# Optimization experiments

Measured on AMD Instinct MI355X. Metric: run time of the kernel, lower is better.

Reference implementation:

```python
import jax, jax.numpy as jnp
import numpy as np

IN_FEATURES = 4096
OUT_FEATURES = 4096
BLOCK_SIZE = 4096
NUM_BLOCKS = 4096
CODEBOOK_SIZE = 256
TOTAL_WEIGHTS = OUT_FEATURES * IN_FEATURES


def setup_inputs() -> dict:
    key = jax.random.key(0)
    k_x, k_cb, k_b, k_idx = jax.random.split(key, 4)
    x = jax.random.normal(k_x, (4, 2048, IN_FEATURES), dtype=jnp.float32)
    codebook = jax.random.normal(k_cb, (NUM_BLOCKS, CODEBOOK_SIZE), dtype=jnp.float32)
    bias = jax.random.normal(k_b, (OUT_FEATURES,), dtype=jnp.float32)
    indices = jax.random.randint(k_idx, (NUM_BLOCKS, BLOCK_SIZE), 0, CODEBOOK_SIZE, dtype=jnp.int64)
    return {"x": x, "codebook": codebook, "bias": bias, "indices": indices}


def reference(x, codebook, bias, indices):
    # weight = codebook[block_idx, indices] : per-block gather of codebook entries
    # codebook: [num_blocks, codebook_size], indices: [num_blocks, block_size]
    w_blocks = jnp.take_along_axis(codebook, indices, axis=1)  # [num_blocks, block_size]
    weight = w_blocks.reshape(-1)[:TOTAL_WEIGHTS].reshape(OUT_FEATURES, IN_FEATURES)
    # F.linear: x @ weight.T + bias
    return jnp.einsum("bsi,oi->bso", x, weight) + bias
```

## Files before the change

kernel.cpp:

```cpp
#include <hip/hip_runtime.h>

typedef __bf16 bf16x8 __attribute__((ext_vector_type(8)));
typedef float f32x4 __attribute__((ext_vector_type(4)));
typedef unsigned short u16x8 __attribute__((ext_vector_type(8)));
typedef int i32x4 __attribute__((ext_vector_type(4)));

#define M_TOT 8192
#define K_TOT 4096
#define N_TOT 4096
#define BM 256
#define BN 256
#define BK 64
#define NT (K_TOT / BK)

__device__ __forceinline__ unsigned short f2bf(float f) {
  union { float f; unsigned int u; } v; v.f = f;
  unsigned int u = v.u;
  return (unsigned short)((u + 0x7FFFu + ((u >> 16) & 1u)) >> 16);
}

__global__ __launch_bounds__(256) void prep(const float* __restrict__ cb,
                                            const int* __restrict__ idx,
                                            const float* __restrict__ X,
                                            unsigned short* __restrict__ Wb,
                                            unsigned short* __restrict__ Xc) {
  const int b = blockIdx.x;
  if (b < 8192) {
    size_t base = ((size_t)b * 256 + threadIdx.x) * 8;
    const float* crow = cb + ((base >> 12) << 8);
    i32x4 i0 = *(const i32x4*)(idx + base);
    i32x4 i1 = *(const i32x4*)(idx + base + 4);
    u16x8 o;
#pragma unroll
    for (int j = 0; j < 4; ++j) { o[j] = f2bf(crow[i0[j]]); o[4 + j] = f2bf(crow[i1[j]]); }
    *(u16x8*)(Wb + base) = o;
  } else {
    size_t base = ((size_t)(b - 8192) * 256 + threadIdx.x) * 8;
    f32x4 a = *(const f32x4*)(X + base);
    f32x4 c = *(const f32x4*)(X + base + 4);
    u16x8 o;
#pragma unroll
    for (int j = 0; j < 4; ++j) { o[j] = f2bf(a[j]); o[4 + j] = f2bf(c[j]); }
    *(u16x8*)(Xc + base) = o;
  }
}

#define GLDS16(g, l)                                                      \
  __builtin_amdgcn_global_load_lds(                                       \
      (__attribute__((address_space(1))) void*)(g),                       \
      (__attribute__((address_space(3))) void*)(l), 16, 0, 0)

__global__ __launch_bounds__(512, 2) void gemm8(const unsigned short* __restrict__ A,
                                                const unsigned short* __restrict__ B,
                                                const float* __restrict__ bias,
                                                float* __restrict__ C) {
  __shared__ __attribute__((aligned(128))) char lds[131072];

  const int tid = threadIdx.x;
  const int lane = tid & 63;
  const int wm = (tid >> 6) >> 2;
  const int wn = (tid >> 6) & 3;
  const int lr = lane & 15;

  const int bid = blockIdx.x;
  const int swz = (bid & 7) * 64 + (bid >> 3);
  const int bm = swz >> 4;
  const int bn = swz & 15;

  const unsigned short* Ap = A + (size_t)bm * BM * K_TOT;
  const unsigned short* Bp = B + (size_t)bn * BN * K_TOT;

  const int srow = tid >> 3;
  const int sgcol = (((tid & 7) * 16) ^ ((srow & 7) << 4)) >> 1;
  const int wavebase = (tid & 448) << 4;

  const int cs0 = (((lane >> 4) << 4)) ^ ((lr & 7) << 4);
  const int cs1 = (64 + ((lane >> 4) << 4)) ^ ((lr & 7) << 4);
  const int rowA0 = (wm * 128 + lr) * 128;
  const int rowB0 = 32768 + (wn * 64 + lr) * 128;

#define RD(off) (*(const bf16x8*)(lds + (off)))
#define STAGE(GB, TK, RB, LOFF)                                               \
  { _Pragma("unroll")                                                         \
    for (int ii = 0; ii < 2; ++ii) {                                          \
      GLDS16((GB) + (size_t)((RB) + ii * 64 + srow) * K_TOT + (TK) + sgcol,   \
             lds + (LOFF) + ii * 8192 + wavebase);                            \
    } }
#define BARRIER()                       \
  {                                     \
    asm volatile("" ::: "memory");      \
    __builtin_amdgcn_s_barrier();       \
    asm volatile("" ::: "memory");      \
  }

#define MFMA_Q(MH, AV, BV)                                                    \
  { __builtin_amdgcn_s_setprio(1);                                            \
    _Pragma("unroll")                                                         \
    for (int r = 0; r < 4; ++r) {                                             \
      _Pragma("unroll")                                                       \
      for (int nf = 0; nf < 4; ++nf)                                          \
        acc[(MH) * 4 + r][nf] = __builtin_amdgcn_mfma_f32_16x16x32_bf16(      \
            AV[r], BV[nf], acc[(MH) * 4 + r][nf], 0, 0, 0);                   \
    }                                                                         \
    __builtin_amdgcn_s_setprio(0); }

#define TILE(T, BO, STG_A, STG_B, VMF, DO_BAR)                                    \
  {                                                                               \
    bf16x8 Aa[4], Ab[4], Ac[4], Ad[4], Bx[4], By[4];                              \
    _Pragma("unroll") for (int r = 0; r < 4; ++r)                                 \
        Aa[r] = RD((BO) + rowA0 + r * 2048 + cs0);                                \
    _Pragma("unroll") for (int n = 0; n < 4; ++n)                                 \
        Bx[n] = RD((BO) + rowB0 + n * 2048 + cs0);                                \
    if (STG_A) STAGE(Ap, ((T) + 1) * BK, 0, ((BO) ^ 65536) + 0);                  \
    _Pragma("unroll") for (int r = 0; r < 4; ++r)                                 \
        Ab[r] = RD((BO) + rowA0 + (4 + r) * 2048 + cs0);                          \
    if (STG_A) STAGE(Ap, ((T) + 1) * BK, 128, ((BO) ^ 65536) + 16384);            \
    MFMA_Q(0, Aa, Bx);                                                            \
    _Pragma("unroll") for (int r = 0; r < 4; ++r)                                 \
        Ac[r] = RD((BO) + rowA0 + r * 2048 + cs1);                                \
    _Pragma("unroll") for (int n = 0; n < 4; ++n)                                 \
        By[n] = RD((BO) + rowB0 + n * 2048 + cs1);                                \
    MFMA_Q(1, Ab, Bx);                                                            \
    asm volatile("s_waitcnt lgkmcnt(0)" ::: "memory");                            \
    BARRIER();                                                                    \
    if (STG_B) STAGE(Bp, ((T) + 2) * BK, 0, (BO) + 32768);                        \
    if (STG_B) STAGE(Bp, ((T) + 2) * BK, 128, (BO) + 49152);                      \
    _Pragma("unroll") for (int r = 0; r < 4; ++r)                                 \
        Ad[r] = RD((BO) + rowA0 + (4 + r) * 2048 + cs1);                          \
    MFMA_Q(0, Ac, By);                                                            \
    MFMA_Q(1, Ad, By);                                                            \
    asm volatile("s_waitcnt vmcnt(" VMF ")" ::: "memory");                        \
    if (DO_BAR) BARRIER();                                                        \
  }

  f32x4 acc[8][4] = {};

  STAGE(Bp, 0, 0, 32768);
  STAGE(Bp, 0, 128, 49152);
  STAGE(Ap, 0, 0, 0);
  STAGE(Ap, 0, 128, 16384);
  STAGE(Bp, BK, 0, 65536 + 32768);
  STAGE(Bp, BK, 128, 65536 + 49152);
  asm volatile("s_waitcnt vmcnt(4)" ::: "memory");
  BARRIER();

  for (int t = 0; t < NT - 2; t += 2) {
    TILE(t,     0,     1, 1, "4", 1);
    TILE(t + 1, 65536, 1, 1, "4", 1);
  }
  TILE(NT - 2, 0,     1, 0, "0", 1);
  TILE(NT - 1, 65536, 0, 0, "0", 0);

  const int lg4 = (lane >> 4) << 2;
#pragma unroll
  for (int nf = 0; nf < 4; ++nf) {
    const int col = bn * BN + wn * 64 + nf * 16 + lr;
    const float bv = bias[col];
#pragma unroll
    for (int mf = 0; mf < 8; ++mf) {
      const int row0 = bm * BM + wm * 128 + mf * 16 + lg4;
      float* cp = C + (size_t)row0 * N_TOT + col;
#pragma unroll
      for (int j = 0; j < 4; ++j) cp[(size_t)j * N_TOT] = acc[mf][nf][j] + bv;
    }
  }
#undef RD
#undef STAGE
#undef BARRIER
#undef MFMA_Q
#undef TILE
}

extern "C" void kernel_launch(void* const* d_in, const int* in_sizes, int n_in,
                              void* d_out, int out_size, void* d_ws, size_t ws_size,
                              hipStream_t stream) {
  const float* x    = (const float*)d_in[0];
  const float* cb   = (const float*)d_in[1];
  const float* bias = (const float*)d_in[2];
  const int*   idx  = (const int*)d_in[3];

  float* out = (float*)d_out;

  unsigned short* Wb = (unsigned short*)d_ws;
  unsigned short* Xc = (unsigned short*)((char*)d_ws + (size_t)N_TOT * K_TOT * 2);

  prep<<<24576, 256, 0, stream>>>(cb, idx, x, Wb, Xc);
  gemm8<<<512, 512, 0, stream>>>(Xc, Wb, bias, out);
}
```

Measured before the change: 275.0 us.

## Restructure GEMM tile into four barrier-fenced quadrant phases with interleaved staging

Reorganizes each K-tile of the bf16 MFMA GEMM into four quadrant phases (M-half x N-half), each loading both K sub-slices of its fragments from LDS, then a barrier-fenced MFMA cluster. Global-to-LDS staging of the next A and B tiles is spread across the phases. The aim is a ping-pong style schedule where the two co-resident workgroups alternate between LDS reads and MFMA bursts, so memory and matrix work overlap. The extra barriers per tile add synchronization overhead, and the register pressure for holding A fragments across phases changes.

```diff
diff --git a/kernel.cpp b/kernel.cpp
--- a/kernel.cpp
+++ b/kernel.cpp
@@ -92,64 +92,84 @@
     __builtin_amdgcn_s_barrier();       \
     asm volatile("" ::: "memory");      \
   }
-
-#define MFMA_Q(MH, AV, BV)                                                    \
+#define LGKM0() asm volatile("s_waitcnt lgkmcnt(0)" ::: "memory")
+
+#define MFMA_Q(MH, NH, AV, BV)                                                \
   { __builtin_amdgcn_s_setprio(1);                                            \
     _Pragma("unroll")                                                         \
     for (int r = 0; r < 4; ++r) {                                             \
       _Pragma("unroll")                                                       \
-      for (int nf = 0; nf < 4; ++nf)                                          \
-        acc[(MH) * 4 + r][nf] = __builtin_amdgcn_mfma_f32_16x16x32_bf16(      \
-            AV[r], BV[nf], acc[(MH) * 4 + r][nf], 0, 0, 0);                   \
+      for (int n2 = 0; n2 < 2; ++n2) {                                        \
+        acc[(MH)*4+r][(NH)*2+n2] = __builtin_amdgcn_mfma_f32_16x16x32_bf16(   \
+            AV[r*2+0], BV[n2*2+0], acc[(MH)*4+r][(NH)*2+n2], 0, 0, 0);        \
+        acc[(MH)*4+r][(NH)*2+n2] = __builtin_amdgcn_mfma_f32_16x16x32_bf16(   \
+            AV[r*2+1], BV[n2*2+1], acc[(MH)*4+r][(NH)*2+n2], 0, 0, 0);        \
+      }                                                                       \
     }                                                                         \
     __builtin_amdgcn_s_setprio(0); }
 
-#define TILE(T, BO, STG_A, STG_B, VMF, DO_BAR)                                    \
+#define TILE(T, BO, STG_A, STG_B, VMF, LAST)                                      \
   {                                                                               \
-    bf16x8 Aa[4], Ab[4], Ac[4], Ad[4], Bx[4], By[4];                              \
-    _Pragma("unroll") for (int r = 0; r < 4; ++r)                                 \
-        Aa[r] = RD((BO) + rowA0 + r * 2048 + cs0);                                \
-    _Pragma("unroll") for (int n = 0; n < 4; ++n)                                 \
-        Bx[n] = RD((BO) + rowB0 + n * 2048 + cs0);                                \
+    bf16x8 Aq[8], A2[8], Bn0[4], Bn1[4];                                          \
+                   \
+    _Pragma("unroll") for (int r = 0; r < 4; ++r) {                               \
+      Aq[r*2+0] = RD((BO) + rowA0 + r * 2048 + cs0);                              \
+      Aq[r*2+1] = RD((BO) + rowA0 + r * 2048 + cs1);                              \
+    }                                                                             \
+    _Pragma("unroll") for (int n = 0; n < 2; ++n) {                               \
+      Bn0[n*2+0] = RD((BO) + rowB0 + n * 2048 + cs0);                             \
+      Bn0[n*2+1] = RD((BO) + rowB0 + n * 2048 + cs1);                             \
+    }                                                                             \
     if (STG_A) STAGE(Ap, ((T) + 1) * BK, 0, ((BO) ^ 65536) + 0);                  \
-    _Pragma("unroll") for (int r = 0; r < 4; ++r)                                 \
-        Ab[r] = RD((BO) + rowA0 + (4 + r) * 2048 + cs0);                          \
+    asm volatile("s_waitcnt lgkmcnt(8)" ::: "memory");                            \
+    BARRIER(); LGKM0();                                                           \
+    MFMA_Q(0, 0, Aq, Bn0);                                                        \
+    BARRIER();                                                                    \
+                               \
+    _Pragma("unroll") for (int n = 0; n < 2; ++n) {                               \
+      Bn1[n*2+0] = RD((BO) + rowB0 + (2 + n) * 2048 + cs0);                       \
+      Bn1[n*2+1] = RD((BO) + rowB0 + (2 + n) * 2048 + cs1);                       \
+    }                                                                             \
     if (STG_A) STAGE(Ap, ((T) + 1) * BK, 128, ((BO) ^ 65536) + 16384);            \
-    MFMA_Q(0, Aa, Bx);                                                            \
-    _Pragma("unroll") for (int r = 0; r < 4; ++r)                                 \
-        Ac[r] = RD((BO) + rowA0 + r * 2048 + cs1);                                \
-    _Pragma("unroll") for (int n = 0; n < 4; ++n)                                 \
-        By[n] = RD((BO) + rowB0 + n * 2048 + cs1);                                \
-    MFMA_Q(1, Ab, Bx);                                                            \
-    asm volatile("s_waitcnt lgkmcnt(0)" ::: "memory");                            \
-    BARRIER();                                                                    \
+    BARRIER(); LGKM0();                                                           \
+    MFMA_Q(0, 1, Aq, Bn1);                                                        \
+    BARRIER();                                                                    \
+         \
+    _Pragma("unroll") for (int r = 0; r < 4; ++r) {                               \
+      A2[r*2+0] = RD((BO) + rowA0 + (4 + r) * 2048 + cs0);                        \
+      A2[r*2+1] = RD((BO) + rowA0 + (4 + r) * 2048 + cs1);                        \
+    }                                                                             \
     if (STG_B) STAGE(Bp, ((T) + 2) * BK, 0, (BO) + 32768);                        \
+    BARRIER(); LGKM0();                                                           \
+    MFMA_Q(1, 0, A2, Bn0);                                                        \
+    BARRIER();                                                                    \
+                      \
     if (STG_B) STAGE(Bp, ((T) + 2) * BK, 128, (BO) + 49152);                      \
-    _Pragma("unroll") for (int r = 0; r < 4; ++r)                                 \
-        Ad[r] = RD((BO) + rowA0 + (4 + r) * 2048 + cs1);                          \
-    MFMA_Q(0, Ac, By);                                                            \
-    MFMA_Q(1, Ad, By);                                                            \
-    asm volatile("s_waitcnt vmcnt(" VMF ")" ::: "memory");                        \
-    if (DO_BAR) BARRIER();                                                        \
+    BARRIER();                                                                    \
+    MFMA_Q(1, 1, A2, Bn1);                                                        \
+    if (!(LAST)) {                                                                \
+      asm volatile("s_waitcnt vmcnt(" VMF ")" ::: "memory");                      \
+      BARRIER();                                                                  \
+    }                                                                             \
   }
 
   f32x4 acc[8][4] = {};
 
+  STAGE(Ap, 0, 0, 0);
+  STAGE(Ap, 0, 128, 16384);
   STAGE(Bp, 0, 0, 32768);
   STAGE(Bp, 0, 128, 49152);
-  STAGE(Ap, 0, 0, 0);
-  STAGE(Ap, 0, 128, 16384);
   STAGE(Bp, BK, 0, 65536 + 32768);
   STAGE(Bp, BK, 128, 65536 + 49152);
   asm volatile("s_waitcnt vmcnt(4)" ::: "memory");
   BARRIER();
 
   for (int t = 0; t < NT - 2; t += 2) {
-    TILE(t,     0,     1, 1, "4", 1);
-    TILE(t + 1, 65536, 1, 1, "4", 1);
-  }
-  TILE(NT - 2, 0,     1, 0, "0", 1);
-  TILE(NT - 1, 65536, 0, 0, "0", 0);
+    TILE(t,     0,     1, 1, "4", 0);
+    TILE(t + 1, 65536, 1, 1, "4", 0);
+  }
+  TILE(NT - 2, 0,     1, 0, "0", 0);
+  TILE(NT - 1, 65536, 0, 0, "0", 1);
 
   const int lg4 = (lane >> 4) << 2;
 #pragma unroll
@@ -167,6 +187,7 @@
 #undef RD
 #undef STAGE
 #undef BARRIER
+#undef LGKM0
 #undef MFMA_Q
 #undef TILE
 }
```

New measurement: 276.9 us. Within noise of the previous version (+0.7%).
